# Kernel tuning notes

Hardware: AMD Instinct MI355X
Metric: run time of the kernel (lower is better)

The kernel has to match this reference:

```python
import jax, jax.numpy as jnp
import numpy as np

B, N, DIM = 64, 197, 768
NUM_HEAD, HEAD_DIM = 12, 64
SCALE = HEAD_DIM ** -0.5
WS = (14, 14)
NUM_REL = (2 * WS[0] - 1) * (2 * WS[1] - 1) + 3  # 732


def _relative_position_index():
    coords = np.stack(np.meshgrid(np.arange(WS[0]), np.arange(WS[1]), indexing='ij'))  # (2, Wh, Ww)
    cf = coords.reshape(2, -1)                              # (2, Wh*Ww)
    rel = (cf[:, :, None] - cf[:, None, :]).transpose(1, 2, 0).astype(np.int64)
    rel[:, :, 0] += WS[0] - 1
    rel[:, :, 1] += WS[1] - 1
    rel[:, :, 0] *= 2 * WS[1] - 1
    idx = np.zeros((WS[0] * WS[1] + 1,) * 2, dtype=np.int32)
    idx[1:, 1:] = rel.sum(-1)
    idx[0, :] = NUM_REL - 3
    idx[:, 0] = NUM_REL - 2
    idx[0, 0] = NUM_REL - 1
    return idx


def setup_inputs() -> dict:
    key = jax.random.key(0)
    k1, k2, k3, k4 = jax.random.split(key, 4)
    x = jax.random.normal(k1, (B, N, DIM), dtype=jnp.float32)
    qkv_w = jax.random.normal(k2, (3 * DIM, DIM), dtype=jnp.float32) * (DIM ** -0.5)
    q_bias = jnp.zeros((DIM,), dtype=jnp.float32)
    v_bias = jnp.zeros((DIM,), dtype=jnp.float32)
    rpb_table = jax.random.normal(k3, (NUM_REL, NUM_HEAD), dtype=jnp.float32) * 0.02
    proj_w = jax.random.normal(k4, (DIM, DIM), dtype=jnp.float32) * (DIM ** -0.5)
    proj_b = jnp.zeros((DIM,), dtype=jnp.float32)
    rel_index = jnp.asarray(_relative_position_index())
    return {"x": x, "qkv_w": qkv_w, "q_bias": q_bias, "v_bias": v_bias,
            "rpb_table": rpb_table, "proj_w": proj_w, "proj_b": proj_b,
            "rel_index": rel_index}


def reference(x, qkv_w, q_bias, v_bias, rpb_table, proj_w, proj_b, rel_index):
    b, n, c = x.shape
    # qkv projection with [q_bias, 0, v_bias] bias layout
    qkv_bias = jnp.concatenate([q_bias, jnp.zeros_like(v_bias), v_bias])
    qkv = x @ qkv_w.T + qkv_bias                               # (B, N, 3*C)
    qkv = qkv.reshape(b, n, 3, NUM_HEAD, HEAD_DIM).transpose(2, 0, 3, 1, 4)
    q, k, v = qkv[0] * SCALE, qkv[1], qkv[2]                   # (B, H, N, hd)
    attn = jnp.einsum('bhqd,bhkd->bhqk', q, k)                 # (B, H, N, N)
    # relative position bias gather: table[(N,N)] -> (N, N, H) -> (H, N, N)
    bias = rpb_table[rel_index].transpose(2, 0, 1)
    attn = jax.nn.softmax(attn + bias[None], axis=-1)
    out = jnp.einsum('bhqk,bhkd->bhqd', attn, v)               # (B, H, N, hd)
    out = out.transpose(0, 2, 1, 3).reshape(b, n, -1)
    return out @ proj_w.T + proj_b
```

## Files before the change

kernel.cpp:

```cpp
#include <hip/hip_runtime.h>


#define B_    64
#define N_    197
#define DIM_  768
#define H_    12
#define HD_   64
#define M_TOT (B_ * N_)

#define ST_A0   0
#define ST_A1   13312
#define ST_A2   26624
#define ST_B0   39936
#define ST_B1   52224
#define ST_B2   64512
#define OFF_Q   0
#define OFF_K   13312
#define OFF_VT  26624
#define LDS_TOT 76800

typedef __attribute__((ext_vector_type(8))) short bf8;
typedef __attribute__((ext_vector_type(4))) float f4;
typedef __attribute__((ext_vector_type(4))) unsigned short us4;

__device__ __forceinline__ unsigned short f2bf(float f) {
    unsigned u = __float_as_uint(f);
    u = (u + 0x7fffu + ((u >> 16) & 1u)) >> 16;
    return (unsigned short)u;
}

__device__ __forceinline__ void gl2lds16(const unsigned short* g, unsigned short* l) {
    __builtin_amdgcn_global_load_lds(
        (const __attribute__((address_space(1))) void*)g,
        (__attribute__((address_space(3))) void*)l, 16, 0, 0);
}

__device__ __forceinline__ int qkaddr(int row, int col) {
    return row * 64 + ((((col >> 3) ^ row) & 7) << 3) + (col & 7);
}
__device__ __forceinline__ int vtaddr(int d, int k) {
    int s = k >> 3;
    int s2 = (s < 24) ? ((s & 24) | ((s ^ d) & 7)) : (24 + ((s ^ d) & 3));
    return d * 224 + (s2 << 3) + (k & 7);
}

__global__ void k_prep(const float* __restrict__ x, const float* __restrict__ qkvw,
                       const float* __restrict__ projw, const float* __restrict__ rpb,
                       const int* __restrict__ relidx,
                       unsigned short* __restrict__ x_bf, unsigned short* __restrict__ qkvw_bf,
                       unsigned short* __restrict__ projw_bf, float* __restrict__ bias_hqk) {
    const int T = gridDim.x * blockDim.x;
    const int tid = blockIdx.x * blockDim.x + threadIdx.x;
    for (int i = tid; i < M_TOT * DIM_ / 4; i += T) {
        float4 v = ((const float4*)x)[i];
        us4 o = {f2bf(v.x), f2bf(v.y), f2bf(v.z), f2bf(v.w)};
        ((us4*)x_bf)[i] = o;
    }
    for (int i = tid; i < 3 * DIM_ * DIM_ / 4; i += T) {
        float4 v = ((const float4*)qkvw)[i];
        us4 o = {f2bf(v.x), f2bf(v.y), f2bf(v.z), f2bf(v.w)};
        ((us4*)qkvw_bf)[i] = o;
    }
    for (int i = tid; i < DIM_ * DIM_ / 4; i += T) {
        float4 v = ((const float4*)projw)[i];
        us4 o = {f2bf(v.x), f2bf(v.y), f2bf(v.z), f2bf(v.w)};
        ((us4*)projw_bf)[i] = o;
    }
    for (int i = tid; i < H_ * N_ * N_; i += T) {
        int h = i / (N_ * N_), qk = i - h * (N_ * N_);
        bias_hqk[i] = rpb[relidx[qk] * H_ + h];
    }
}

__global__ __launch_bounds__(1024) void k_fused(const unsigned short* __restrict__ X,
                                                const unsigned short* __restrict__ Wqkv,
                                                const float* __restrict__ qb,
                                                const float* __restrict__ vbias,
                                                const float* __restrict__ bias_hqk,
                                                unsigned short* __restrict__ att_ws) {
    __shared__ unsigned short lds[LDS_TOT];

    const int t = threadIdx.x;
    const int w = t >> 6, lane = t & 63, ln = lane & 15, quad = lane >> 4;
    const int wm = w >> 2, wn = w & 3;
    const int srl = lane >> 3;
    const int src8 = (lane & 7) ^ srl;

    const int gid = blockIdx.x;
    const int local = gid >> 3;
    const int b = (gid & 7) * 8 + (local & 7);
    const int h = local >> 3;

    const unsigned short* xb = X + (size_t)b * 197 * 768;

    auto stage = [&](int kt, int aOfs, int bOfs) {
#pragma unroll
        for (int i = 0; i < 4; ++i) {
            int idx = (15 - w) + 16 * i;
            if (idx >= 50) break;
            if (idx < 26) {
                int tok = 8 * idx + srl;
                if (tok > 196) tok = 196;
                gl2lds16(xb + (size_t)tok * 768 + kt * 64 + src8 * 8,
                         &lds[aOfs + idx * 512]);
            } else {
                int bb = idx - 26;
                int rr = 8 * bb + srl;
                gl2lds16(Wqkv + (size_t)((rr >> 6) * 768 + h * 64 + (rr & 63)) * 768
                              + kt * 64 + src8 * 8,
                         &lds[bOfs + bb * 512]);
            }
        }
    };

    f4 acc[4][3] = {};

    auto compute = [&](int aOfs, int bOfs) {
#pragma unroll
        for (int ks = 0; ks < 2; ++ks) {
            bf8 bfr[3];
#pragma unroll
            for (int tl = 0; tl < 3; ++tl) {
                int rr = (wn * 3 + tl) * 16 + ln;
                int slot = (ks * 4 + quad) ^ (rr & 7);
                bfr[tl] = *(const bf8*)&lds[bOfs + rr * 64 + slot * 8];
            }
            __builtin_amdgcn_s_setprio(1);
#pragma unroll
            for (int mi = 0; mi < 4; ++mi) {
                int mt = wm + 4 * mi;
                if (mt >= 13) continue;
                int row = mt * 16 + ln;
                int slot = (ks * 4 + quad) ^ (row & 7);
                bf8 af = *(const bf8*)&lds[aOfs + row * 64 + slot * 8];
#pragma unroll
                for (int tl = 0; tl < 3; ++tl)
                    acc[mi][tl] = __builtin_amdgcn_mfma_f32_16x16x32_bf16(
                        af, bfr[tl], acc[mi][tl], 0, 0, 0);
            }
            __builtin_amdgcn_s_setprio(0);
        }
    };

    const int stA[3] = {ST_A0, ST_A1, ST_A2};
    const int stB[3] = {ST_B0, ST_B1, ST_B2};
    stage(0, ST_A0, ST_B0);
    stage(1, ST_A1, ST_B1);
#pragma unroll
    for (int kt = 0; kt < 12; ++kt) {
        if (kt < 11) { __asm__ __volatile__("s_waitcnt vmcnt(3)" ::: "memory"); }
        else         { __asm__ __volatile__("s_waitcnt vmcnt(0)" ::: "memory"); }
        __builtin_amdgcn_sched_barrier(0);
        __builtin_amdgcn_s_barrier();
        __builtin_amdgcn_sched_barrier(0);
        if (kt + 2 < 12) stage(kt + 2, stA[(kt + 2) % 3], stB[(kt + 2) % 3]);
        compute(stA[kt % 3], stB[kt % 3]);
    }
    __syncthreads();

#pragma unroll
    for (int tl = 0; tl < 3; ++tl) {
        int tn = wn * 3 + tl;
        int p = tn >> 2;
        int col = (tn & 3) * 16 + ln;
        int d = h * 64 + col;
        float bj = (p == 0) ? qb[d] : (p == 2) ? vbias[d] : 0.0f;
#pragma unroll
        for (int mi = 0; mi < 4; ++mi) {
            int mt = wm + 4 * mi;
            if (mt >= 13) continue;
#pragma unroll
            for (int r = 0; r < 4; ++r) {
                int row = mt * 16 + quad * 4 + r;
                float v = acc[mi][tl][r];
                if (p == 0)      lds[OFF_Q + qkaddr(row, col)] = f2bf((v + bj) * 0.125f);
                else if (p == 1) lds[OFF_K + qkaddr(row, col)] = f2bf(v);
                else             lds[OFF_VT + vtaddr(col, row)] = f2bf(v + bj);
            }
        }
    }
    for (int idx = t; idx < 64 * 16; idx += 1024) {
        int d = idx >> 4, k = 208 + (idx & 15);
        lds[OFF_VT + vtaddr(d, k)] = 0;
    }
    __syncthreads();

    const float* bp = bias_hqk + (size_t)h * 197 * 197;

    for (int mt = w; mt < 13; mt += 16) {
        bf8 qa[2];
#pragma unroll
        for (int ks = 0; ks < 2; ++ks)
            qa[ks] = *(const bf8*)&lds[OFF_Q + qkaddr(mt * 16 + ln, ks * 32 + quad * 8)];

        f4 sacc[13];
#pragma unroll
        for (int nt = 0; nt < 13; ++nt) sacc[nt] = (f4){0.f, 0.f, 0.f, 0.f};
        __builtin_amdgcn_s_setprio(1);
#pragma unroll
        for (int nt = 0; nt < 13; ++nt) {
#pragma unroll
            for (int ks = 0; ks < 2; ++ks) {
                bf8 ka = *(const bf8*)&lds[OFF_K + qkaddr(nt * 16 + ln, ks * 32 + quad * 8)];
                sacc[nt] = __builtin_amdgcn_mfma_f32_16x16x32_bf16(ka, qa[ks], sacc[nt], 0, 0, 0);
            }
        }
        __builtin_amdgcn_s_setprio(0);

        int qg = mt * 16 + ln;
        const float* brow = bp + (size_t)(qg < 197 ? qg : 196) * 197;
        float mx = -3.0e38f;
#pragma unroll
        for (int nt = 0; nt < 13; ++nt)
#pragma unroll
            for (int r = 0; r < 4; ++r) {
                int kg = nt * 16 + quad * 4 + r;
                float s = (kg < 197) ? (sacc[nt][r] + brow[kg]) : -3.0e38f;
                sacc[nt][r] = s;
                mx = fmaxf(mx, s);
            }
        mx = fmaxf(mx, __shfl_xor(mx, 16, 64));
        mx = fmaxf(mx, __shfl_xor(mx, 32, 64));
        float sum = 0.f;
#pragma unroll
        for (int nt = 0; nt < 13; ++nt)
#pragma unroll
            for (int r = 0; r < 4; ++r) {
                float pv = __expf(sacc[nt][r] - mx);
                sacc[nt][r] = pv;
                sum += pv;
            }
        sum += __shfl_xor(sum, 16, 64);
        sum += __shfl_xor(sum, 32, 64);
        float inv = 1.0f / sum;

        unsigned pk[14][2];
#pragma unroll
        for (int nt = 0; nt < 13; ++nt) {
            pk[nt][0] = (unsigned)f2bf(sacc[nt][0] * inv) |
                        ((unsigned)f2bf(sacc[nt][1] * inv) << 16);
            pk[nt][1] = (unsigned)f2bf(sacc[nt][2] * inv) |
                        ((unsigned)f2bf(sacc[nt][3] * inv) << 16);
        }
        pk[13][0] = 0; pk[13][1] = 0;

        const int sA = (((lane & 15) | ((lane & 16) << 1)) << 2);
        const int sB = sA + 64;
        const bool hi = (lane & 32) != 0;
        f4 o[4];
#pragma unroll
        for (int j = 0; j < 4; ++j) o[j] = (f4){0.f, 0.f, 0.f, 0.f};
#pragma unroll
        for (int ks = 0; ks < 7; ++ks) {
            int b0 = __builtin_amdgcn_ds_bpermute(sA, (int)pk[2 * ks][0]);
            int b1 = __builtin_amdgcn_ds_bpermute(sA, (int)pk[2 * ks][1]);
            int b2 = __builtin_amdgcn_ds_bpermute(sB, (int)pk[2 * ks][0]);
            int b3 = __builtin_amdgcn_ds_bpermute(sB, (int)pk[2 * ks][1]);
            int c0 = __builtin_amdgcn_ds_bpermute(sA, (int)pk[2 * ks + 1][0]);
            int c1 = __builtin_amdgcn_ds_bpermute(sA, (int)pk[2 * ks + 1][1]);
            int c2 = __builtin_amdgcn_ds_bpermute(sB, (int)pk[2 * ks + 1][0]);
            int c3 = __builtin_amdgcn_ds_bpermute(sB, (int)pk[2 * ks + 1][1]);
            union { int u[4]; bf8 v; } uu;
            uu.u[0] = hi ? c0 : b0;
            uu.u[1] = hi ? c1 : b1;
            uu.u[2] = hi ? c2 : b2;
            uu.u[3] = hi ? c3 : b3;
            __builtin_amdgcn_s_setprio(1);
#pragma unroll
            for (int j = 0; j < 4; ++j) {
                bf8 vf = *(const bf8*)&lds[OFF_VT + vtaddr(j * 16 + ln, ks * 32 + quad * 8)];
                o[j] = __builtin_amdgcn_mfma_f32_16x16x32_bf16(uu.v, vf, o[j], 0, 0, 0);
            }
            __builtin_amdgcn_s_setprio(0);
        }
#pragma unroll
        for (int j = 0; j < 4; ++j)
#pragma unroll
            for (int r = 0; r < 4; ++r) {
                int tok = mt * 16 + quad * 4 + r;
                if (tok < 197)
                    att_ws[((size_t)b * 197 + tok) * 768 + h * 64 + j * 16 + ln] = f2bf(o[j][r]);
            }
    }
}

__device__ __forceinline__ void pj_stage(const unsigned short* __restrict__ A,
                                         const unsigned short* __restrict__ Bm,
                                         int bm, int bn, int kt, int w, int rsub, int src8,
                                         unsigned short* a_l, unsigned short* b_l) {
#pragma unroll
    for (int c = 0; c < 4; ++c) {
        int rb = w * 32 + c * 8;
        int gr = bm * 128 + rb + rsub;
        if (gr > M_TOT - 1) gr = M_TOT - 1;
        gl2lds16(A + (size_t)gr * 768 + kt * 64 + (src8 << 3), &a_l[rb * 64]);
        int gc = bn * 128 + rb + rsub;
        gl2lds16(Bm + (size_t)gc * 768 + kt * 64 + (src8 << 3), &b_l[rb * 64]);
    }
}

__device__ __forceinline__ void pj_compute(const unsigned short* a_l, const unsigned short* b_l,
                                           int wm, int wn, int ln, int quad, f4 (*acc)[4]) {
#pragma unroll
    for (int ks = 0; ks < 2; ++ks) {
        bf8 af[4], bfr[4];
#pragma unroll
        for (int i = 0; i < 4; ++i)
            af[i] = *(const bf8*)&a_l[((wm * 64 + i * 16 + ln) << 6) +
                                      ((((ks << 2) + quad) ^ (ln & 7)) << 3)];
#pragma unroll
        for (int j = 0; j < 4; ++j)
            bfr[j] = *(const bf8*)&b_l[((wn * 64 + j * 16 + ln) << 6) +
                                       ((((ks << 2) + quad) ^ (ln & 7)) << 3)];
#pragma unroll
        for (int i = 0; i < 4; ++i)
#pragma unroll
            for (int j = 0; j < 4; ++j)
                acc[i][j] = __builtin_amdgcn_mfma_f32_16x16x32_bf16(af[i], bfr[j], acc[i][j], 0, 0, 0);
    }
}

__global__ __launch_bounds__(256) void k_proj(const unsigned short* __restrict__ A,
                                              const unsigned short* __restrict__ Bm,
                                              const float* __restrict__ pb,
                                              float* __restrict__ out) {
    __shared__ unsigned short a0[128 * 64], a1[128 * 64];
    __shared__ unsigned short b0[128 * 64], b1[128 * 64];
    const int t = threadIdx.x;
    const int w = t >> 6, lane = t & 63, ln = lane & 15, quad = lane >> 4;
    const int wm = w & 1, wn = w >> 1;

    const int gid = blockIdx.x;
    const int panel = gid / 48, rem = gid - panel * 48;
    const int pm0 = panel * 8;
    const int psz = (99 - pm0 < 8) ? (99 - pm0) : 8;
    const int bm = pm0 + rem % psz;
    const int bn = rem / psz;

    const int rsub = lane >> 3;
    const int src8 = (lane & 7) ^ rsub;

    f4 acc[4][4] = {};

    pj_stage(A, Bm, bm, bn, 0, w, rsub, src8, a0, b0);
#pragma unroll
    for (int kt = 0; kt < 12; ++kt) {
        __asm__ __volatile__("s_waitcnt vmcnt(0)" ::: "memory");
        __builtin_amdgcn_sched_barrier(0);
        __builtin_amdgcn_s_barrier();
        __builtin_amdgcn_sched_barrier(0);
        if (kt + 1 < 12) pj_stage(A, Bm, bm, bn, kt + 1, w, rsub, src8,
                                  (kt & 1) ? a0 : a1, (kt & 1) ? b0 : b1);
        pj_compute((kt & 1) ? a1 : a0, (kt & 1) ? b1 : b0, wm, wn, ln, quad, acc);
    }

#pragma unroll
    for (int i = 0; i < 4; ++i) {
#pragma unroll
        for (int r = 0; r < 4; ++r) {
            int row_g = bm * 128 + wm * 64 + i * 16 + quad * 4 + r;
            if (row_g >= M_TOT) continue;
#pragma unroll
            for (int j = 0; j < 4; ++j) {
                int col_g = bn * 128 + wn * 64 + j * 16 + ln;
                out[(size_t)row_g * 768 + col_g] = acc[i][j][r] + pb[col_g];
            }
        }
    }
}

extern "C" void kernel_launch(void* const* d_in, const int* in_sizes, int n_in,
                              void* d_out, int out_size, void* d_ws, size_t ws_size,
                              hipStream_t stream) {
    const float* x     = (const float*)d_in[0];
    const float* qkvw  = (const float*)d_in[1];
    const float* qb    = (const float*)d_in[2];
    const float* vb    = (const float*)d_in[3];
    const float* rpb   = (const float*)d_in[4];
    const float* projw = (const float*)d_in[5];
    const float* pb    = (const float*)d_in[6];
    const int*   ridx  = (const int*)d_in[7];
    float* out = (float*)d_out;

    char* ws = (char*)d_ws;
    size_t off = 0;
    auto alloc = [&](size_t bytes) -> void* {
        void* p = ws + off;
        off = (off + bytes + 255) & ~(size_t)255;
        return p;
    };
    unsigned short* x_bf     = (unsigned short*)alloc((size_t)M_TOT * DIM_ * 2);
    unsigned short* qkvw_bf  = (unsigned short*)alloc((size_t)3 * DIM_ * DIM_ * 2);
    unsigned short* projw_bf = (unsigned short*)alloc((size_t)DIM_ * DIM_ * 2);
    float*          bias_h   = (float*)alloc((size_t)H_ * N_ * N_ * 4);
    unsigned short* att_ws   = (unsigned short*)alloc((size_t)(M_TOT + 64) * DIM_ * 2);
    (void)ws_size; (void)in_sizes; (void)n_in; (void)out_size;

    k_prep<<<1200, 256, 0, stream>>>(x, qkvw, projw, rpb, ridx,
                                     x_bf, qkvw_bf, projw_bf, bias_h);
    k_fused<<<768, 1024, 0, stream>>>(x_bf, qkvw_bf, qb, vb, bias_h, att_ws);
    k_proj<<<594, 256, 0, stream>>>(att_ws, projw_bf, pb, out);
}
```

Measured before the change: 211.5 us.

## Triple-buffer projection GEMM with K=32 stages and prefetch depth two

Restructures the output projection GEMM pipeline. It shrinks each K-tile from 64 to 32 and uses a 3-slot LDS ring with two stages in flight, waiting with a partial vmcnt instead of draining all loads. It also shrinks LDS use so three blocks can share a CU, sets launch_bounds occupancy to 3, and raises wave priority around the MFMA burst. In exchange there are twice as many barriers per tile and a new swizzled layout packing two rows per 64-element LDS line, which must match the gather pattern.

```diff
diff --git a/kernel.cpp b/kernel.cpp
--- a/kernel.cpp
+++ b/kernel.cpp
@@ -284,48 +284,56 @@
     }
 }
 
+#define PJ_BUF 8192
+
 __device__ __forceinline__ void pj_stage(const unsigned short* __restrict__ A,
                                          const unsigned short* __restrict__ Bm,
-                                         int bm, int bn, int kt, int w, int rsub, int src8,
-                                         unsigned short* a_l, unsigned short* b_l) {
-#pragma unroll
-    for (int c = 0; c < 4; ++c) {
-        int rb = w * 32 + c * 8;
-        int gr = bm * 128 + rb + rsub;
+                                         int bm, int bn, int kt, int w, int srl, int src8,
+                                         unsigned short* buf) {
+#pragma unroll
+    for (int i = 0; i < 2; ++i) {
+        int idx = w * 2 + i;
+        int gr = bm * 128 + 2 * (idx * 8 + srl) + (src8 >> 2);
         if (gr > M_TOT - 1) gr = M_TOT - 1;
-        gl2lds16(A + (size_t)gr * 768 + kt * 64 + (src8 << 3), &a_l[rb * 64]);
-        int gc = bn * 128 + rb + rsub;
-        gl2lds16(Bm + (size_t)gc * 768 + kt * 64 + (src8 << 3), &b_l[rb * 64]);
-    }
-}
-
-__device__ __forceinline__ void pj_compute(const unsigned short* a_l, const unsigned short* b_l,
+        gl2lds16(A + (size_t)gr * 768 + kt * 32 + (src8 & 3) * 8,
+                 &buf[idx * 512]);
+        int gc = bn * 128 + 2 * (idx * 8 + srl) + (src8 >> 2);
+        gl2lds16(Bm + (size_t)gc * 768 + kt * 32 + (src8 & 3) * 8,
+                 &buf[4096 + idx * 512]);
+    }
+}
+
+__device__ __forceinline__ void pj_compute(const unsigned short* buf,
                                            int wm, int wn, int ln, int quad, f4 (*acc)[4]) {
-#pragma unroll
-    for (int ks = 0; ks < 2; ++ks) {
-        bf8 af[4], bfr[4];
-#pragma unroll
-        for (int i = 0; i < 4; ++i)
-            af[i] = *(const bf8*)&a_l[((wm * 64 + i * 16 + ln) << 6) +
-                                      ((((ks << 2) + quad) ^ (ln & 7)) << 3)];
+    bf8 af[4], bfr[4];
+#pragma unroll
+    for (int i = 0; i < 4; ++i) {
+        int row = wm * 64 + i * 16 + ln;
+        int sr = row >> 1;
+        int slot = (((row & 1) << 2) | quad) ^ (sr & 7);
+        af[i] = *(const bf8*)&buf[sr * 64 + slot * 8];
+    }
+#pragma unroll
+    for (int j = 0; j < 4; ++j) {
+        int row = wn * 64 + j * 16 + ln;
+        int sr = row >> 1;
+        int slot = (((row & 1) << 2) | quad) ^ (sr & 7);
+        bfr[j] = *(const bf8*)&buf[4096 + sr * 64 + slot * 8];
+    }
+    __builtin_amdgcn_s_setprio(1);
+#pragma unroll
+    for (int i = 0; i < 4; ++i)
 #pragma unroll
         for (int j = 0; j < 4; ++j)
-            bfr[j] = *(const bf8*)&b_l[((wn * 64 + j * 16 + ln) << 6) +
-                                       ((((ks << 2) + quad) ^ (ln & 7)) << 3)];
-#pragma unroll
-        for (int i = 0; i < 4; ++i)
-#pragma unroll
-            for (int j = 0; j < 4; ++j)
-                acc[i][j] = __builtin_amdgcn_mfma_f32_16x16x32_bf16(af[i], bfr[j], acc[i][j], 0, 0, 0);
-    }
-}
-
-__global__ __launch_bounds__(256) void k_proj(const unsigned short* __restrict__ A,
-                                              const unsigned short* __restrict__ Bm,
-                                              const float* __restrict__ pb,
-                                              float* __restrict__ out) {
-    __shared__ unsigned short a0[128 * 64], a1[128 * 64];
-    __shared__ unsigned short b0[128 * 64], b1[128 * 64];
+            acc[i][j] = __builtin_amdgcn_mfma_f32_16x16x32_bf16(af[i], bfr[j], acc[i][j], 0, 0, 0);
+    __builtin_amdgcn_s_setprio(0);
+}
+
+__global__ __launch_bounds__(256, 3) void k_proj(const unsigned short* __restrict__ A,
+                                                 const unsigned short* __restrict__ Bm,
+                                                 const float* __restrict__ pb,
+                                                 float* __restrict__ out) {
+    __shared__ unsigned short plds[3 * PJ_BUF];
     const int t = threadIdx.x;
     const int w = t >> 6, lane = t & 63, ln = lane & 15, quad = lane >> 4;
     const int wm = w & 1, wn = w >> 1;
@@ -337,21 +345,23 @@
     const int bm = pm0 + rem % psz;
     const int bn = rem / psz;
 
-    const int rsub = lane >> 3;
-    const int src8 = (lane & 7) ^ rsub;
+    const int srl = lane >> 3;
+    const int src8 = (lane & 7) ^ srl;
 
     f4 acc[4][4] = {};
 
-    pj_stage(A, Bm, bm, bn, 0, w, rsub, src8, a0, b0);
-#pragma unroll
-    for (int kt = 0; kt < 12; ++kt) {
-        __asm__ __volatile__("s_waitcnt vmcnt(0)" ::: "memory");
+    pj_stage(A, Bm, bm, bn, 0, w, srl, src8, &plds[0]);
+    pj_stage(A, Bm, bm, bn, 1, w, srl, src8, &plds[PJ_BUF]);
+#pragma unroll
+    for (int kt = 0; kt < 24; ++kt) {
+        if (kt < 23) { __asm__ __volatile__("s_waitcnt vmcnt(4)" ::: "memory"); }
+        else         { __asm__ __volatile__("s_waitcnt vmcnt(0)" ::: "memory"); }
         __builtin_amdgcn_sched_barrier(0);
         __builtin_amdgcn_s_barrier();
         __builtin_amdgcn_sched_barrier(0);
-        if (kt + 1 < 12) pj_stage(A, Bm, bm, bn, kt + 1, w, rsub, src8,
-                                  (kt & 1) ? a0 : a1, (kt & 1) ? b0 : b1);
-        pj_compute((kt & 1) ? a1 : a0, (kt & 1) ? b1 : b0, wm, wn, ln, quad, acc);
+        if (kt + 2 < 24) pj_stage(A, Bm, bm, bn, kt + 2, w, srl, src8,
+                                  &plds[((kt + 2) % 3) * PJ_BUF]);
+        pj_compute(&plds[(kt % 3) * PJ_BUF], wm, wn, ln, quad, acc);
     }
 
 #pragma unroll
```

New measurement: 207.9 us (median of 2 runs). No clear change (-1.7%).
